# Kernel tuning notes

Measured on AMD Instinct MI355X. Metric: run time of the kernel, lower is better.

## Reference

```python
import jax, jax.numpy as jnp
import numpy as np

B, I, C, H, W = 8, 16, 256, 64, 64  # batch, instances, channels(=in=out), spatial


def setup_inputs() -> dict:
    key = jax.random.key(0)
    ks = jax.random.split(key, 8)
    x = jax.random.normal(ks[0], (B, C, H, W), dtype=jnp.float32)
    masks = jax.random.uniform(ks[1], (B, I, H, W), dtype=jnp.float32)
    # conv_feat: 1x1 conv C->C  -> weight [C_out, C_in]
    Wf = jax.random.normal(ks[2], (C, C), dtype=jnp.float32) * 0.02
    bf = jax.random.normal(ks[3], (C,), dtype=jnp.float32) * 0.02
    # conv_mask: grouped 1x1 conv, groups=I, each 1 -> C channels -> weight [I, C]
    Wm = jax.random.normal(ks[4], (I, C), dtype=jnp.float32) * 0.02
    bm = jax.random.normal(ks[5], (I, C), dtype=jnp.float32) * 0.02
    # conv_out: 1x1 conv C->C
    Wo = jax.random.normal(ks[6], (C, C), dtype=jnp.float32) * 0.02
    bo = jax.random.normal(ks[7], (C,), dtype=jnp.float32) * 0.02
    gamma = jnp.float32(0.5)  # torch init is 0.0; use nonzero so baseline is nontrivial
    return {"x": x, "masks": masks, "Wf": Wf, "bf": bf, "Wm": Wm, "bm": bm,
            "Wo": Wo, "bo": bo, "gamma": gamma}


def reference(x, masks, Wf, bf, Wm, bm, Wo, bo, gamma):
    b, i, h, w = masks.shape
    c = Wf.shape[0]
    # conv_feat: 1x1 conv == per-pixel matmul
    feat = jnp.einsum('bchw,oc->bohw', x, Wf) + bf[:, None, None]  # [B,C,H,W]
    # grouped 1x1 conv_mask: instance i channel -> C channels
    mc = (masks[:, :, None, :, :] * Wm[None, :, :, None, None]
          + bm[None, :, :, None, None])                              # [B,I,C,H,W]
    # softmax over (C*H*W) per instance, as in masks.view(B, I, -1)
    mc = jax.nn.softmax(mc.reshape(b, i, -1), axis=-1).reshape(b, i, c, h, w)
    # loop sum_i conv_out(feat * mask_i)  ==  conv_out_W @ (feat * sum_i mask_i) + I*bias
    msum = mc.sum(axis=1)                                            # [B,C,H,W]
    out = jnp.einsum('bchw,oc->bohw', feat * msum, Wo) + (i * bo)[:, None, None]
    return gamma * out + x
```

## Files before the change

kernel.cpp:

```cpp
#include <hip/hip_runtime.h>


#define NB 8
#define NI 16
#define NC 256
#define HWSZ 4096
#define PT 64

typedef __attribute__((ext_vector_type(8))) short short8;
typedef __attribute__((ext_vector_type(4))) short short4v;
typedef __attribute__((ext_vector_type(4))) float f32x4;

static __device__ inline short f2bf(float f) {
    unsigned u = __builtin_bit_cast(unsigned, f);
    u += 0x7fffu + ((u >> 16) & 1u);
    return (short)(u >> 16);
}
static __device__ inline float bf2f(short h) {
    unsigned u = ((unsigned)(unsigned short)h) << 16;
    return __builtin_bit_cast(float, u);
}

__global__ __launch_bounds__(256)
void setup_kernel(const float* __restrict__ masks, const float* __restrict__ Wm,
                  const float* __restrict__ bm, const float* __restrict__ Wf,
                  const float* __restrict__ Wo, short* __restrict__ Ahat,
                  short* __restrict__ WfB, short* __restrict__ WoB) {
    const int blk = blockIdx.x, t = threadIdx.x;
    if (blk >= NB * NI) {
        const int wb = blk - NB * NI;
#pragma unroll
        for (int r = 0; r < 2; ++r) {
            int fid = (wb * 256 + t) * 2 + r;
            const float* src = (fid < 16384) ? Wf : Wo;
            short* dst       = (fid < 16384) ? WfB : WoB;
            int e = (fid & 16383) * 4;
            float4 v = *(const float4*)(src + e);
            short4v o = { f2bf(v.x), f2bf(v.y), f2bf(v.z), f2bf(v.w) };
            *(short4v*)(dst + e) = o;
        }
        return;
    }
    const int bi = blk;
    const int b  = bi >> 4;
    const int i  = bi & (NI - 1);
    const float* m = masks + (size_t)bi * HWSZ;

    float s1 = 0.f, s2 = 0.f, s3 = 0.f, s4 = 0.f, s5 = 0.f, s6 = 0.f;
    for (int e = t; e < HWSZ; e += 256) {
        float v = m[e];
        float v2 = v * v, v3 = v2 * v;
        s1 += v; s2 += v2; s3 += v3;
        s4 += v2 * v2; s5 += v2 * v3; s6 += v3 * v3;
    }
    __shared__ float red[7][4];
    float sv[6] = { s1, s2, s3, s4, s5, s6 };
#pragma unroll
    for (int k = 0; k < 6; ++k) {
        float v = sv[k];
#pragma unroll
        for (int off = 32; off > 0; off >>= 1) v += __shfl_down(v, off, 64);
        if ((t & 63) == 0) red[k][t >> 6] = v;
    }
    __syncthreads();
    const float S1 = red[0][0] + red[0][1] + red[0][2] + red[0][3];
    const float S2 = red[1][0] + red[1][1] + red[1][2] + red[1][3];
    const float S3 = red[2][0] + red[2][1] + red[2][2] + red[2][3];
    const float S4 = red[3][0] + red[3][1] + red[3][2] + red[3][3];
    const float S5 = red[4][0] + red[4][1] + red[4][2] + red[4][3];
    const float S6 = red[5][0] + red[5][1] + red[5][2] + red[5][3];

    const int c = t;
    const float w  = Wm[i * NC + c];
    const float eb = __expf(bm[i * NC + c]);
    const float poly = (float)HWSZ
        + w * (S1 + w * (0.5f * S2 + w * ((1.f / 6.f) * S3
        + w * ((1.f / 24.f) * S4 + w * ((1.f / 120.f) * S5
        + w * ((1.f / 720.f) * S6))))));
    float v = eb * poly;
#pragma unroll
    for (int off = 32; off > 0; off >>= 1) v += __shfl_down(v, off, 64);
    if ((t & 63) == 0) red[6][t >> 6] = v;
    __syncthreads();
    const float Z = red[6][0] + red[6][1] + red[6][2] + red[6][3];
    const float a = eb / Z;
    short4v av = { f2bf(a), f2bf(a * w), f2bf(a * w * w * 0.5f),
                   f2bf(a * w * w * w * (1.f / 6.f)) };
    *(short4v*)(Ahat + ((size_t)(b * NC + c)) * 64 + i * 4) = av;
}

__global__ __launch_bounds__(256, 2)
void main_kernel(const float* __restrict__ x, const float* __restrict__ masks,
                 const float* __restrict__ bf_, const float* __restrict__ bo,
                 const float* __restrict__ gamma_p,
                 const short* __restrict__ WfB, const short* __restrict__ WoB,
                 const short* __restrict__ Ahat, float* __restrict__ out) {
    const int blk  = blockIdx.x;
    const int b    = blk >> 6;
    const int hw0  = (blk & 63) << 6;
    const int t    = threadIdx.x;
    const int lane = t & 63;
    const int ln15 = lane & 15;
    const int q    = lane >> 4;
    const int wo0  = (t >> 6) << 6;

    __shared__ __align__(16) short sA[16896];
    __shared__ __align__(16) short sM[4608];
    __shared__ __align__(16) short sZ[16896];

    const float* xb = x + ((size_t)b * NC) * HWSZ + hw0;

#pragma unroll
    for (int it = 0; it < 4; ++it) {
        int i = (t >> 6) + it * 4;
        int p = t & 63;
        float m = masks[((size_t)(b * NI + i)) * HWSZ + hw0 + p];
        float m2 = m * m;
        short4v mv = { (short)0x3F80, f2bf(m), f2bf(m2), f2bf(m2 * m) };
        *(short4v*)(sM + p * 72 + i * 4) = mv;
    }

    float* F = (float*)sZ;
    float4 xr[4];
#pragma unroll
    for (int it = 0; it < 4; ++it) {
        int idx = it * 256 + t;
        int c = idx >> 4, qf = idx & 15;
        xr[it] = *(const float4*)(xb + (size_t)c * HWSZ + qf * 4);
    }
    for (int s = 0; s < 4; ++s) {
        float* Fb = F + (s & 1) * 4160;
#pragma unroll
        for (int it = 0; it < 4; ++it) {
            int idx = it * 256 + t;
            int c = idx >> 4, qf = idx & 15;
            Fb[c * 65 + qf * 4 + 0] = xr[it].x;
            Fb[c * 65 + qf * 4 + 1] = xr[it].y;
            Fb[c * 65 + qf * 4 + 2] = xr[it].z;
            Fb[c * 65 + qf * 4 + 3] = xr[it].w;
        }
        if (s < 3) {
#pragma unroll
            for (int it = 0; it < 4; ++it) {
                int idx = it * 256 + t;
                int c = idx >> 4, qf = idx & 15;
                xr[it] = *(const float4*)(xb + (size_t)((s + 1) * 64 + c) * HWSZ + qf * 4);
            }
        }
        __syncthreads();
#pragma unroll
        for (int it2 = 0; it2 < 2; ++it2) {
            int idx = it2 * 256 + t;
            int p = idx >> 3, g = idx & 7;
            short8 o8;
#pragma unroll
            for (int j = 0; j < 8; ++j) o8[j] = f2bf(Fb[(g * 8 + j) * 65 + p]);
            *(short8*)(sA + p * 264 + s * 64 + g * 8) = o8;
        }
    }
    __syncthreads();

    f32x4 macc[4][4];
#pragma unroll
    for (int ot = 0; ot < 4; ++ot)
#pragma unroll
        for (int pt = 0; pt < 4; ++pt) macc[ot][pt] = (f32x4)0.f;
    const short* Ab = Ahat + ((size_t)b * NC) * 64;
#pragma unroll
    for (int ks = 0; ks < 2; ++ks) {
        short8 af[4], bfr[4];
#pragma unroll
        for (int ot = 0; ot < 4; ++ot)
            af[ot] = *(const short8*)(Ab + (wo0 + ot * 16 + ln15) * 64 + ks * 32 + q * 8);
#pragma unroll
        for (int pt = 0; pt < 4; ++pt)
            bfr[pt] = *(const short8*)(sM + (pt * 16 + ln15) * 72 + ks * 32 + q * 8);
#pragma unroll
        for (int ot = 0; ot < 4; ++ot)
#pragma unroll
            for (int pt = 0; pt < 4; ++pt)
                macc[ot][pt] = __builtin_amdgcn_mfma_f32_16x16x32_bf16(
                    af[ot], bfr[pt], macc[ot][pt], 0, 0, 0);
    }

    f32x4 feat[4][4];
#pragma unroll
    for (int ot = 0; ot < 4; ++ot)
#pragma unroll
        for (int pt = 0; pt < 4; ++pt) feat[ot][pt] = (f32x4)0.f;
#pragma unroll 2
    for (int ks = 0; ks < 8; ++ks) {
        short8 af[4], bfr[4];
#pragma unroll
        for (int ot = 0; ot < 4; ++ot)
            af[ot] = *(const short8*)(WfB + (wo0 + ot * 16 + ln15) * NC + ks * 32 + q * 8);
#pragma unroll
        for (int pt = 0; pt < 4; ++pt)
            bfr[pt] = *(const short8*)(sA + (pt * 16 + ln15) * 264 + ks * 32 + q * 8);
#pragma unroll
        for (int ot = 0; ot < 4; ++ot)
#pragma unroll
            for (int pt = 0; pt < 4; ++pt)
                feat[ot][pt] = __builtin_amdgcn_mfma_f32_16x16x32_bf16(
                    af[ot], bfr[pt], feat[ot][pt], 0, 0, 0);
    }

#pragma unroll
    for (int ot = 0; ot < 4; ++ot) {
        float4 bv = *(const float4*)(bf_ + wo0 + ot * 16 + q * 4);
        float b4[4] = { bv.x, bv.y, bv.z, bv.w };
#pragma unroll
        for (int pt = 0; pt < 4; ++pt) {
            short4v zz;
#pragma unroll
            for (int r = 0; r < 4; ++r)
                zz[r] = f2bf((feat[ot][pt][r] + b4[r]) * macc[ot][pt][r]);
            *(short4v*)(sZ + (pt * 16 + ln15) * 264 + wo0 + ot * 16 + q * 4) = zz;
        }
    }
    __syncthreads();

    f32x4 oacc[4][4];
#pragma unroll
    for (int ot = 0; ot < 4; ++ot)
#pragma unroll
        for (int pt = 0; pt < 4; ++pt) oacc[ot][pt] = (f32x4)0.f;
#pragma unroll 2
    for (int ks = 0; ks < 8; ++ks) {
        short8 af[4], bfr[4];
#pragma unroll
        for (int ot = 0; ot < 4; ++ot)
            af[ot] = *(const short8*)(WoB + (wo0 + ot * 16 + ln15) * NC + ks * 32 + q * 8);
#pragma unroll
        for (int pt = 0; pt < 4; ++pt)
            bfr[pt] = *(const short8*)(sZ + (pt * 16 + ln15) * 264 + ks * 32 + q * 8);
#pragma unroll
        for (int ot = 0; ot < 4; ++ot)
#pragma unroll
            for (int pt = 0; pt < 4; ++pt)
                oacc[ot][pt] = __builtin_amdgcn_mfma_f32_16x16x32_bf16(
                    af[ot], bfr[pt], oacc[ot][pt], 0, 0, 0);
    }

    __syncthreads();
#pragma unroll
    for (int ot = 0; ot < 4; ++ot)
#pragma unroll
        for (int pt = 0; pt < 4; ++pt)
#pragma unroll
            for (int r = 0; r < 4; ++r)
                sA[(wo0 + ot * 16 + q * 4 + r) * 68 + pt * 16 + ln15] =
                    f2bf(oacc[ot][pt][r]);
    __syncthreads();

    const float g = gamma_p[0];
    float* ob = out + ((size_t)b * NC) * HWSZ + hw0;
#pragma unroll 4
    for (int it = 0; it < 16; ++it) {
        int idx = it * 256 + t;
        int o = idx >> 4, pq = idx & 15;
        short4v zb = *(const short4v*)(sA + o * 68 + pq * 4);
        float bov = 16.0f * bo[o];
        float4 xv = *(const float4*)(xb + (size_t)o * HWSZ + pq * 4);
        float4 r;
        r.x = g * (bf2f(zb[0]) + bov) + xv.x;
        r.y = g * (bf2f(zb[1]) + bov) + xv.y;
        r.z = g * (bf2f(zb[2]) + bov) + xv.z;
        r.w = g * (bf2f(zb[3]) + bov) + xv.w;
        *(float4*)(ob + (size_t)o * HWSZ + pq * 4) = r;
    }
}

extern "C" void kernel_launch(void* const* d_in, const int* in_sizes, int n_in,
                              void* d_out, int out_size, void* d_ws, size_t ws_size,
                              hipStream_t stream) {
    const float* x     = (const float*)d_in[0];
    const float* masks = (const float*)d_in[1];
    const float* Wf    = (const float*)d_in[2];
    const float* bf    = (const float*)d_in[3];
    const float* Wm    = (const float*)d_in[4];
    const float* bm    = (const float*)d_in[5];
    const float* Wo    = (const float*)d_in[6];
    const float* bo    = (const float*)d_in[7];
    const float* gamma = (const float*)d_in[8];
    float* out = (float*)d_out;

    short* ws   = (short*)d_ws;
    short* WfB  = ws;
    short* WoB  = WfB + NC * NC;
    short* Ahat = WoB + NC * NC;

    hipLaunchKernelGGL(setup_kernel, dim3(NB * NI + 64), dim3(256), 0, stream,
                       masks, Wm, bm, Wf, Wo, Ahat, WfB, WoB);
    hipLaunchKernelGGL(main_kernel, dim3(NB * (HWSZ / PT)), dim3(256), 0, stream,
                       x, masks, bf, bo, gamma, WfB, WoB, Ahat, out);
}
```

Measured before the change: 126.3 us.

## Halve pixel tile to 32, shrink shared memory, raise occupancy to four blocks

```diff
diff --git a/kernel.cpp b/kernel.cpp
--- a/kernel.cpp
+++ b/kernel.cpp
@@ -5,7 +5,7 @@
 #define NI 16
 #define NC 256
 #define HWSZ 4096
-#define PT 64
+#define PT 32
 
 typedef __attribute__((ext_vector_type(8))) short short8;
 typedef __attribute__((ext_vector_type(4))) short short4v;
@@ -89,118 +89,100 @@
     *(short4v*)(Ahat + ((size_t)(b * NC + c)) * 64 + i * 4) = av;
 }
 
-__global__ __launch_bounds__(256, 2)
+__global__ __launch_bounds__(256, 4)
 void main_kernel(const float* __restrict__ x, const float* __restrict__ masks,
                  const float* __restrict__ bf_, const float* __restrict__ bo,
                  const float* __restrict__ gamma_p,
                  const short* __restrict__ WfB, const short* __restrict__ WoB,
                  const short* __restrict__ Ahat, float* __restrict__ out) {
     const int blk  = blockIdx.x;
-    const int b    = blk >> 6;
-    const int hw0  = (blk & 63) << 6;
+    const int b    = blk >> 7;
+    const int hw0  = (blk & 127) << 5;
     const int t    = threadIdx.x;
     const int lane = t & 63;
     const int ln15 = lane & 15;
     const int q    = lane >> 4;
-    const int wo0  = (t >> 6) << 6;
-
-    __shared__ __align__(16) short sA[16896];
-    __shared__ __align__(16) short sM[4608];
-    __shared__ __align__(16) short sZ[16896];
-
-    const float* xb = x + ((size_t)b * NC) * HWSZ + hw0;
-
-#pragma unroll
-    for (int it = 0; it < 4; ++it) {
-        int i = (t >> 6) + it * 4;
-        int p = t & 63;
-        float m = masks[((size_t)(b * NI + i)) * HWSZ + hw0 + p];
-        float m2 = m * m;
-        short4v mv = { (short)0x3F80, f2bf(m), f2bf(m2), f2bf(m2 * m) };
-        *(short4v*)(sM + p * 72 + i * 4) = mv;
-    }
-
-    float* F = (float*)sZ;
-    float4 xr[4];
-#pragma unroll
-    for (int it = 0; it < 4; ++it) {
-        int idx = it * 256 + t;
-        int c = idx >> 4, qf = idx & 15;
-        xr[it] = *(const float4*)(xb + (size_t)c * HWSZ + qf * 4);
-    }
-    for (int s = 0; s < 4; ++s) {
-        float* Fb = F + (s & 1) * 4160;
-#pragma unroll
-        for (int it = 0; it < 4; ++it) {
-            int idx = it * 256 + t;
-            int c = idx >> 4, qf = idx & 15;
-            Fb[c * 65 + qf * 4 + 0] = xr[it].x;
-            Fb[c * 65 + qf * 4 + 1] = xr[it].y;
-            Fb[c * 65 + qf * 4 + 2] = xr[it].z;
-            Fb[c * 65 + qf * 4 + 3] = xr[it].w;
+    const int w    = t >> 6;
+    const int wo0  = w << 6;
+
+    __shared__ __align__(16) short smem[19200];
+    short* sA = smem;
+    short* sM = smem + 8448;
+    short* sZ = smem + 10752;
+
+    const float* xbase = x + ((size_t)b * NC) * HWSZ + hw0;
+
+    {
+        const int i  = t >> 4;
+        const int p2 = (t & 15) * 2;
+        const float* mp = masks + ((size_t)(b * NI + i)) * HWSZ + hw0 + p2;
+        float m0 = mp[0], m1 = mp[1];
+        float m0s = m0 * m0, m1s = m1 * m1;
+        short4v v0 = { (short)0x3F80, f2bf(m0), f2bf(m0s), f2bf(m0s * m0) };
+        short4v v1 = { (short)0x3F80, f2bf(m1), f2bf(m1s), f2bf(m1s * m1) };
+        *(short4v*)(sM + p2 * 72 + i * 4) = v0;
+        *(short4v*)(sM + (p2 + 1) * 72 + i * 4) = v1;
+    }
+
+    {
+        const int pk = lane & 31;
+        const int g  = lane >> 5;
+#pragma unroll
+        for (int s = 0; s < 4; ++s) {
+            const int cb = s * 64 + w * 16 + g * 8;
+            const float* src = xbase + (size_t)cb * HWSZ + pk;
+            float v[8];
+#pragma unroll
+            for (int j = 0; j < 8; ++j) v[j] = src[(size_t)j * HWSZ];
+            short8 o8;
+#pragma unroll
+            for (int j = 0; j < 8; ++j) o8[j] = f2bf(v[j]);
+            *(short8*)(sA + pk * 264 + cb) = o8;
         }
-        if (s < 3) {
-#pragma unroll
-            for (int it = 0; it < 4; ++it) {
-                int idx = it * 256 + t;
-                int c = idx >> 4, qf = idx & 15;
-                xr[it] = *(const float4*)(xb + (size_t)((s + 1) * 64 + c) * HWSZ + qf * 4);
-            }
-        }
-        __syncthreads();
-#pragma unroll
-        for (int it2 = 0; it2 < 2; ++it2) {
-            int idx = it2 * 256 + t;
-            int p = idx >> 3, g = idx & 7;
-            short8 o8;
-#pragma unroll
-            for (int j = 0; j < 8; ++j) o8[j] = f2bf(Fb[(g * 8 + j) * 65 + p]);
-            *(short8*)(sA + p * 264 + s * 64 + g * 8) = o8;
-        }
-    }
-    __syncthreads();
-
-    f32x4 macc[4][4];
-#pragma unroll
-    for (int ot = 0; ot < 4; ++ot)
-#pragma unroll
-        for (int pt = 0; pt < 4; ++pt) macc[ot][pt] = (f32x4)0.f;
+    }
+    __syncthreads();
+
+    f32x4 macc[4][2];
+#pragma unroll
+    for (int ot = 0; ot < 4; ++ot)
+#pragma unroll
+        for (int pt = 0; pt < 2; ++pt) macc[ot][pt] = (f32x4)0.f;
     const short* Ab = Ahat + ((size_t)b * NC) * 64;
 #pragma unroll
     for (int ks = 0; ks < 2; ++ks) {
-        short8 af[4], bfr[4];
+        short8 af[4], bfr[2];
 #pragma unroll
         for (int ot = 0; ot < 4; ++ot)
             af[ot] = *(const short8*)(Ab + (wo0 + ot * 16 + ln15) * 64 + ks * 32 + q * 8);
 #pragma unroll
-        for (int pt = 0; pt < 4; ++pt)
+        for (int pt = 0; pt < 2; ++pt)
             bfr[pt] = *(const short8*)(sM + (pt * 16 + ln15) * 72 + ks * 32 + q * 8);
 #pragma unroll
         for (int ot = 0; ot < 4; ++ot)
 #pragma unroll
-            for (int pt = 0; pt < 4; ++pt)
+            for (int pt = 0; pt < 2; ++pt)
                 macc[ot][pt] = __builtin_amdgcn_mfma_f32_16x16x32_bf16(
                     af[ot], bfr[pt], macc[ot][pt], 0, 0, 0);
     }
 
-    f32x4 feat[4][4];
-#pragma unroll
-    for (int ot = 0; ot < 4; ++ot)
-#pragma unroll
-        for (int pt = 0; pt < 4; ++pt) feat[ot][pt] = (f32x4)0.f;
+    f32x4 feat[4][2];
+#pragma unroll
+    for (int ot = 0; ot < 4; ++ot)
+#pragma unroll
+        for (int pt = 0; pt < 2; ++pt) feat[ot][pt] = (f32x4)0.f;
 #pragma unroll 2
     for (int ks = 0; ks < 8; ++ks) {
-        short8 af[4], bfr[4];
+        short8 af[4], bfr[2];
 #pragma unroll
         for (int ot = 0; ot < 4; ++ot)
             af[ot] = *(const short8*)(WfB + (wo0 + ot * 16 + ln15) * NC + ks * 32 + q * 8);
 #pragma unroll
-        for (int pt = 0; pt < 4; ++pt)
+        for (int pt = 0; pt < 2; ++pt)
             bfr[pt] = *(const short8*)(sA + (pt * 16 + ln15) * 264 + ks * 32 + q * 8);
 #pragma unroll
         for (int ot = 0; ot < 4; ++ot)
 #pragma unroll
-            for (int pt = 0; pt < 4; ++pt)
+            for (int pt = 0; pt < 2; ++pt)
                 feat[ot][pt] = __builtin_amdgcn_mfma_f32_16x16x32_bf16(
                     af[ot], bfr[pt], feat[ot][pt], 0, 0, 0);
     }
@@ -210,7 +192,7 @@
         float4 bv = *(const float4*)(bf_ + wo0 + ot * 16 + q * 4);
         float b4[4] = { bv.x, bv.y, bv.z, bv.w };
 #pragma unroll
-        for (int pt = 0; pt < 4; ++pt) {
+        for (int pt = 0; pt < 2; ++pt) {
             short4v zz;
 #pragma unroll
             for (int r = 0; r < 4; ++r)
@@ -220,48 +202,47 @@
     }
     __syncthreads();
 
-    f32x4 oacc[4][4];
-#pragma unroll
-    for (int ot = 0; ot < 4; ++ot)
-#pragma unroll
-        for (int pt = 0; pt < 4; ++pt) oacc[ot][pt] = (f32x4)0.f;
+    f32x4 oacc[4][2];
+#pragma unroll
+    for (int ot = 0; ot < 4; ++ot)
+#pragma unroll
+        for (int pt = 0; pt < 2; ++pt) oacc[ot][pt] = (f32x4)0.f;
 #pragma unroll 2
     for (int ks = 0; ks < 8; ++ks) {
-        short8 af[4], bfr[4];
+        short8 af[4], bfr[2];
 #pragma unroll
         for (int ot = 0; ot < 4; ++ot)
             af[ot] = *(const short8*)(WoB + (wo0 + ot * 16 + ln15) * NC + ks * 32 + q * 8);
 #pragma unroll
-        for (int pt = 0; pt < 4; ++pt)
+        for (int pt = 0; pt < 2; ++pt)
             bfr[pt] = *(const short8*)(sZ + (pt * 16 + ln15) * 264 + ks * 32 + q * 8);
 #pragma unroll
         for (int ot = 0; ot < 4; ++ot)
 #pragma unroll
-            for (int pt = 0; pt < 4; ++pt)
+            for (int pt = 0; pt < 2; ++pt)
                 oacc[ot][pt] = __builtin_amdgcn_mfma_f32_16x16x32_bf16(
                     af[ot], bfr[pt], oacc[ot][pt], 0, 0, 0);
     }
 
-    __syncthreads();
-#pragma unroll
-    for (int ot = 0; ot < 4; ++ot)
-#pragma unroll
-        for (int pt = 0; pt < 4; ++pt)
+#pragma unroll
+    for (int ot = 0; ot < 4; ++ot)
+#pragma unroll
+        for (int pt = 0; pt < 2; ++pt)
 #pragma unroll
             for (int r = 0; r < 4; ++r)
-                sA[(wo0 + ot * 16 + q * 4 + r) * 68 + pt * 16 + ln15] =
+                smem[(wo0 + ot * 16 + q * 4 + r) * 36 + pt * 16 + ln15] =
                     f2bf(oacc[ot][pt][r]);
     __syncthreads();
 
     const float g = gamma_p[0];
     float* ob = out + ((size_t)b * NC) * HWSZ + hw0;
-#pragma unroll 4
-    for (int it = 0; it < 16; ++it) {
+#pragma unroll
+    for (int it = 0; it < 8; ++it) {
         int idx = it * 256 + t;
-        int o = idx >> 4, pq = idx & 15;
-        short4v zb = *(const short4v*)(sA + o * 68 + pq * 4);
+        int o = idx >> 3, pq = idx & 7;
+        short4v zb = *(const short4v*)(smem + o * 36 + pq * 4);
         float bov = 16.0f * bo[o];
-        float4 xv = *(const float4*)(xb + (size_t)o * HWSZ + pq * 4);
+        float4 xv = *(const float4*)(xbase + (size_t)o * HWSZ + pq * 4);
         float4 r;
         r.x = g * (bf2f(zb[0]) + bov) + xv.x;
         r.y = g * (bf2f(zb[1]) + bov) + xv.y;
```

New measurement: 138.3 us. 1.09x slower.
